# Kernel tuning notes

Measured on AMD Instinct MI355X. Metric: run time of the kernel, lower is better.

## Reference

```python
import jax, jax.numpy as jnp
import numpy as np

D_MODEL = 1024
NUM_HEADS = 16
HEAD_DIM = D_MODEL // NUM_HEADS


def setup_inputs() -> dict:
    key = jax.random.key(0)
    ks = jax.random.split(key, 5)
    s = 0.02
    x = jax.random.normal(ks[0], (4, 2048, D_MODEL), dtype=jnp.float32)
    W_Q = jax.random.normal(ks[1], (D_MODEL, D_MODEL), dtype=jnp.float32) * s
    W_K = jax.random.normal(ks[2], (D_MODEL, D_MODEL), dtype=jnp.float32) * s
    W_V = jax.random.normal(ks[3], (D_MODEL, D_MODEL), dtype=jnp.float32) * s
    W_O = jax.random.normal(ks[4], (D_MODEL, D_MODEL), dtype=jnp.float32) * s
    return {"x": x, "W_Q": W_Q, "W_K": W_K, "W_V": W_V, "W_O": W_O}


def reference(x, W_Q, W_K, W_V, W_O):
    b, s, d = x.shape
    h, hd = NUM_HEADS, HEAD_DIM
    scale = 1.0 / np.sqrt(hd).astype(np.float32)
    # nn.Linear applies x @ W.T; split heads then transpose -> (b, h, s, hd)
    def split(W):
        return (x @ W.T).reshape(b, s, h, hd).transpose(0, 2, 1, 3)
    Q, K, V = split(W_Q), split(W_K), split(W_V)
    scores = jnp.einsum('bhqd,bhkd->bhqk', Q, K) * scale
    causal = jnp.triu(jnp.ones((s, s), dtype=bool), k=1)
    scores = jnp.where(causal, -jnp.inf, scores)
    weights = jax.nn.softmax(scores, axis=-1)
    ctx = jnp.einsum('bhqk,bhkd->bhqd', weights, V)
    ctx = ctx.transpose(0, 2, 1, 3).reshape(b, s, d)
    return ctx @ W_O.T
```

## Files before the change

### kernel.cpp

```cpp
#include <hip/hip_runtime.h>


#define B_  4
#define S_  2048
#define D_  1024
#define H_  16
#define HD_ 64

typedef __attribute__((ext_vector_type(8))) short bf16x8;
typedef __attribute__((ext_vector_type(4))) float f32x4;

#define MFMA16 __builtin_amdgcn_mfma_f32_16x16x32_bf16

__device__ __forceinline__ unsigned short f2b(float f) {
  unsigned u = __builtin_bit_cast(unsigned, f);
  unsigned r = (u + 0x7FFFu + ((u >> 16) & 1u)) >> 16;
  return (unsigned short)r;
}

__device__ __forceinline__ unsigned cvtpk(float lo, float hi) {
  unsigned r;
  asm("v_cvt_pk_bf16_f32 %0, %1, %2" : "=v"(r) : "v"(lo), "v"(hi));
  return r;
}

__device__ __forceinline__ void gll16(const void* g, const void* l) {
  __builtin_amdgcn_global_load_lds(
      (const __attribute__((address_space(1))) unsigned int*)g,
      (__attribute__((address_space(3))) unsigned int*)l, 16, 0, 0);
}

__global__ __launch_bounds__(256) void cvt_all(
    const float4* __restrict__ x,  const float4* __restrict__ wq,
    const float4* __restrict__ wk, const float4* __restrict__ wv,
    const float4* __restrict__ wo,
    ushort4* __restrict__ xb,  ushort4* __restrict__ wqb,
    ushort4* __restrict__ wkb, ushort4* __restrict__ wvb,
    ushort4* __restrict__ wob)
{
  const int y = blockIdx.y;
  const float4* in; ushort4* out;
  if (y < 8)       { in = x  + (size_t)y * 262144; out = xb  + (size_t)y * 262144; }
  else if (y == 8) { in = wq; out = wqb; }
  else if (y == 9) { in = wk; out = wkb; }
  else if (y == 10){ in = wv; out = wvb; }
  else             { in = wo; out = wob; }
  int i = blockIdx.x * 256 + threadIdx.x;
  float4 v = in[i];
  ushort4 o;
  o.x = f2b(v.x); o.y = f2b(v.y); o.z = f2b(v.z); o.w = f2b(v.w);
  out[i] = o;
}

#define GSTG(BF, K0) { \
    _Pragma("unroll") for (int t = 0; t < 2; ++t) { \
      const int grow_ = t*64 + w*16 + srow; \
      const int lbas_ = (t*256 + w*64) * 8; \
      gll16(A + (size_t)(arow + grow_)*1024 + (K0) + scol, &As[BF][lbas_]); \
      gll16(W + (size_t)(brow + grow_)*1024 + (K0) + scol, &Bs[BF][lbas_]); } }

#define GSTEP(BF, SW) { \
    bf16x8 af[4], bfr[4]; \
    _Pragma("unroll") for (int i = 0; i < 4; ++i) \
      af[i]  = *(const bf16x8*)(&As[BF][(wm*64 + i*16 + r16)*32 + rslot]); \
    _Pragma("unroll") for (int i = 0; i < 4; ++i) \
      bfr[i] = *(const bf16x8*)(&Bs[BF][(wn*64 + i*16 + r16)*32 + rslot]); \
    _Pragma("unroll") for (int i = 0; i < 4; ++i) \
      _Pragma("unroll") for (int j = 0; j < 4; ++j) \
        acc[i][j] = (SW) ? MFMA16(bfr[j], af[i], acc[i][j], 0, 0, 0) \
                         : MFMA16(af[i], bfr[j], acc[i][j], 0, 0, 0); }

#define GLOOP(SW) \
  for (int kt = 0; kt < 32; kt += 2) { \
    __syncthreads(); \
    GSTG(1, (kt + 1) * 32); \
    GSTEP(0, SW); \
    __syncthreads(); \
    if (kt + 2 < 32) GSTG(0, (kt + 2) * 32); \
    GSTEP(1, SW); \
  }

template<int MODE>
__global__ __launch_bounds__(256) void gemm_bt(
    const unsigned short* __restrict__ A,
    const unsigned short* __restrict__ W,
    unsigned short* __restrict__ OQ,
    unsigned short* __restrict__ OK,
    unsigned short* __restrict__ OV,
    float* __restrict__ OF)
{
  const int tid  = threadIdx.x;
  const int lane = tid & 63;
  const int w    = tid >> 6;
  const int wm   = w >> 1, wn = w & 1;
  const int r16  = lane & 15, g = lane >> 4;

  const int orig = blockIdx.x + 64 * blockIdx.y;
  const int t_   = orig >> 3;
  const int bm   = (orig & 7) * 8 + (t_ & 7);
  const int bn   = t_ >> 3;

  __shared__ unsigned short As[2][4096];
  __shared__ unsigned short Bs[2][4096];

  const int arow = bm * 128, brow = bn * 128;
  const int srow = lane >> 2;
  const int scol  = ((lane & 3) ^ ((lane >> 3) & 3)) * 8;
  const int rslot = (g ^ ((r16 >> 1) & 3)) * 8;

  f32x4 acc[4][4] = {};
  const bool vblk = (MODE == 0) && (bn >= 16);
  GSTG(0, 0);
  if (!vblk) { GLOOP(true) } else { GLOOP(false) }

  if (MODE == 1) {
    #pragma unroll
    for (int i = 0; i < 4; ++i)
      #pragma unroll
      for (int j = 0; j < 4; ++j) {
        int t = arow + wm*64 + i*16 + r16;
        int f = brow + wn*64 + j*16 + g*4;
        float4 st;
        st.x = acc[i][j][0]; st.y = acc[i][j][1];
        st.z = acc[i][j][2]; st.w = acc[i][j][3];
        *(float4*)(&OF[(size_t)t * 1024 + f]) = st;
      }
  } else if (!vblk) {
    unsigned short* Od = (bn < 8) ? OQ : OK;
    const float scl = (bn < 8) ? 0.18033688f : 1.0f;
    #pragma unroll
    for (int i = 0; i < 4; ++i)
      #pragma unroll
      for (int j = 0; j < 4; ++j) {
        int t = arow + wm*64 + i*16 + r16;
        int f = (brow & 1023) + wn*64 + j*16 + g*4;
        int b = t >> 11, s = t & 2047, h = f >> 6, hd = f & 63;
        uint2 cw;
        cw.x = cvtpk(acc[i][j][0] * scl, acc[i][j][1] * scl);
        cw.y = cvtpk(acc[i][j][2] * scl, acc[i][j][3] * scl);
        *(uint2*)(&Od[((((size_t)b*H_ + h)*S_) + s)*HD_ + hd]) = cw;
      }
  } else {
    #pragma unroll
    for (int i = 0; i < 4; ++i)
      #pragma unroll
      for (int j = 0; j < 4; ++j) {
        int t0 = arow + wm*64 + i*16 + g*4;
        int f  = (brow & 1023) + wn*64 + j*16 + r16;
        int b = t0 >> 11, s = t0 & 2047, h = f >> 6, hd = f & 63;
        uint2 cw;
        cw.x = cvtpk(acc[i][j][0], acc[i][j][1]);
        cw.y = cvtpk(acc[i][j][2], acc[i][j][3]);
        *(uint2*)(&OV[(((size_t)b*H_ + h)*HD_ + hd)*S_ + s]) = cw;
      }
  }
}

#define ASTG(BF, KB) { \
    gll16(Kh + (size_t)((KB) + tr0 +     rsub)*HD_ + csw, &KVb[BF][0][ tr0     *64]); \
    gll16(Kh + (size_t)((KB) + tr0 + 8 + rsub)*HD_ + csw, &KVb[BF][0][(tr0 + 8)*64]); \
    gll16(Vh + (size_t)(tr0 +     rsub)*S_ + (KB) + csw,  &KVb[BF][1][ tr0     *64]); \
    gll16(Vh + (size_t)(tr0 + 8 + rsub)*S_ + (KB) + csw,  &KVb[BF][1][(tr0 + 8)*64]); }

#define ACOMP2(BF, KB) { \
    const int kb_ = (KB); \
    if (kb_ <= qw + 31) { \
      f32x4 sc[2][4]; \
      __builtin_amdgcn_s_setprio(1); \
      _Pragma("unroll") for (int c = 0; c < 4; ++c) { \
        bf16x8 kf0 = *(const bf16x8*)((const char*)&KVb[BF][0][0] + (c*16 + r16)*128 + ((( g      ^ (r16 & 7)) & 7) << 4)); \
        bf16x8 kf1 = *(const bf16x8*)((const char*)&KVb[BF][0][0] + (c*16 + r16)*128 + ((((4 + g) ^ (r16 & 7)) & 7) << 4)); \
        _Pragma("unroll") for (int qi = 0; qi < 2; ++qi) { \
          f32x4 s_ = {}; \
          s_ = MFMA16(kf0, qf[qi][0], s_, 0, 0, 0); \
          s_ = MFMA16(kf1, qf[qi][1], s_, 0, 0, 0); \
          sc[qi][c] = s_; } } \
      __builtin_amdgcn_s_setprio(0); \
      _Pragma("unroll") for (int qi = 0; qi < 2; ++qi) { \
        f32x4 p4[4]; \
        if (kb_ + 63 > qw + qi*16) { \
          const int qrow_ = qw + qi*16 + r16; \
          _Pragma("unroll") for (int c = 0; c < 4; ++c) \
            _Pragma("unroll") for (int r = 0; r < 4; ++r) \
              p4[c][r] = (kb_ + c*16 + g*4 + r > qrow_) ? 0.f : exp2f(sc[qi][c][r]); \
        } else { \
          _Pragma("unroll") for (int c = 0; c < 4; ++c) \
            _Pragma("unroll") for (int r = 0; r < 4; ++r) \
              p4[c][r] = exp2f(sc[qi][c][r]); } \
        char* prp_ = Plw + (qi*16 + r16)*128; \
        const int swz_ = (r16 & 7) << 4; \
        _Pragma("unroll") for (int c = 0; c < 4; ++c) { \
          uint2 pw_; \
          pw_.x = cvtpk(p4[c][0], p4[c][1]); \
          pw_.y = cvtpk(p4[c][2], p4[c][3]); \
          *(uint2*)(prp_ + ((c*32 + g*8) ^ swz_)) = pw_; } } \
      __builtin_amdgcn_s_setprio(1); \
      _Pragma("unroll") for (int kc = 0; kc < 2; ++kc) { \
        bf16x8 pf0_ = *(const bf16x8*)(Plw + r16*128        + ((kc*64 + g*16) ^ ((r16 & 7) << 4))); \
        bf16x8 pf1_ = *(const bf16x8*)(Plw + (16 + r16)*128 + ((kc*64 + g*16) ^ ((r16 & 7) << 4))); \
        oL[0] = MFMA16(onesf, pf0_, oL[0], 0, 0, 0); \
        oL[1] = MFMA16(onesf, pf1_, oL[1], 0, 0, 0); \
        _Pragma("unroll") for (int dn = 0; dn < 4; ++dn) { \
          bf16x8 vf_ = *(const bf16x8*)((const char*)&KVb[BF][1][0] + (dn*16 + r16)*128 + ((((kc*4 + g) ^ (r16 & 7)) & 7) << 4)); \
          oT[0][dn] = MFMA16(vf_, pf0_, oT[0][dn], 0, 0, 0); \
          oT[1][dn] = MFMA16(vf_, pf1_, oT[1][dn], 0, 0, 0); } } \
      __builtin_amdgcn_s_setprio(0); \
    } }

__global__ __launch_bounds__(256, 3) void attn_fwd(
    const unsigned short* __restrict__ Q,
    const unsigned short* __restrict__ K,
    const unsigned short* __restrict__ Vt,
    unsigned short* __restrict__ C)
{
  const int tid  = threadIdx.x;
  const int lane = tid & 63;
  const int w    = tid >> 6;
  const int r16  = lane & 15, g = lane >> 4;

  const int l_   = blockIdx.x;
  const int bh   = (l_ & 7) * 8 + ((l_ >> 3) & 7);
  const int jt   = 15 - (l_ >> 6);
  const int bb   = bh >> 4, hh = bh & 15;

  const unsigned short* Qh = Q  + (size_t)bh * S_ * HD_;
  const unsigned short* Kh = K  + (size_t)bh * S_ * HD_;
  const unsigned short* Vh = Vt + (size_t)bh * HD_ * S_;

  __shared__ unsigned short KVb[2][2][4096];
  __shared__ unsigned short Pl[4][2048];
  char* Plw = (char*)&Pl[w][0];

  const int rsub = lane >> 3;
  const int csw  = ((lane & 7) ^ rsub) * 8;
  const int tr0  = w * 16;

  bf16x8 onesf;
  #pragma unroll
  for (int j = 0; j < 8; ++j) onesf[j] = (short)0x3F80;

  const int q0 = jt * 128;
  const int qw = q0 + w * 32;
  const int nt = 2 * jt + 2;

  bf16x8 qf[2][2];
  #pragma unroll
  for (int qi = 0; qi < 2; ++qi)
    #pragma unroll
    for (int dh = 0; dh < 2; ++dh)
      qf[qi][dh] = *(const bf16x8*)(&Qh[(size_t)(qw + qi*16 + r16) * HD_ + dh*32 + g*8]);

  f32x4 oT[2][4] = {};
  f32x4 oL[2] = {};

  ASTG(0, 0);

  for (int kt = 0; kt < nt; kt += 2) {
    __syncthreads();
    ASTG(1, (kt + 1) * 64);
    ACOMP2(0, kt * 64);
    __syncthreads();
    if (kt + 2 < nt) ASTG(0, (kt + 2) * 64);
    ACOMP2(1, (kt + 1) * 64);
  }

  #pragma unroll
  for (int qi = 0; qi < 2; ++qi) {
    float inv = 1.0f / oL[qi][0];
    int tok = bb * S_ + qw + qi*16 + r16;
    #pragma unroll
    for (int dn = 0; dn < 4; ++dn) {
      uint2 cw;
      cw.x = cvtpk(oT[qi][dn][0] * inv, oT[qi][dn][1] * inv);
      cw.y = cvtpk(oT[qi][dn][2] * inv, oT[qi][dn][3] * inv);
      *(uint2*)(&C[(size_t)tok * D_ + hh*HD_ + dn*16 + g*4]) = cw;
    }
  }
}

extern "C" void kernel_launch(void* const* d_in, const int* in_sizes, int n_in,
                              void* d_out, int out_size, void* d_ws, size_t ws_size,
                              hipStream_t stream) {
  const float* x  = (const float*)d_in[0];
  const float* Wq = (const float*)d_in[1];
  const float* Wk = (const float*)d_in[2];
  const float* Wv = (const float*)d_in[3];
  const float* Wo = (const float*)d_in[4];

  char* ws = (char*)d_ws;
  unsigned short* xb  = (unsigned short*)(ws);
  unsigned short* Wqb = (unsigned short*)(ws + 16777216);
  unsigned short* Wkb = (unsigned short*)(ws + 18874368);
  unsigned short* Wvb = (unsigned short*)(ws + 20971520);
  unsigned short* Wob = (unsigned short*)(ws + 23068672);
  unsigned short* Qb  = (unsigned short*)(ws + 25165824);
  unsigned short* Kb  = (unsigned short*)(ws + 41943040);
  unsigned short* Vtb = (unsigned short*)(ws + 58720256);
  unsigned short* Cb  = (unsigned short*)(ws + 75497472);

  cvt_all<<<dim3(1024, 12), 256, 0, stream>>>(
      (const float4*)x, (const float4*)Wq, (const float4*)Wk,
      (const float4*)Wv, (const float4*)Wo,
      (ushort4*)xb, (ushort4*)Wqb, (ushort4*)Wkb, (ushort4*)Wvb, (ushort4*)Wob);

  gemm_bt<0><<<dim3(64, 24), 256, 0, stream>>>(xb, Wqb, Qb, Kb, Vtb, nullptr);
  attn_fwd<<<1024, 256, 0, stream>>>(Qb, Kb, Vtb, Cb);
  gemm_bt<1><<<dim3(64, 8), 256, 0, stream>>>(Cb, Wob, nullptr, nullptr, nullptr,
                                              (float*)d_out);
}
```

Before: 169.0 us.

## Replace QKV projection with 256x256-tile 8-wave pipelined GEMM kernel

The QKV projection moves to a new kernel with 256x256 output tiles, 512 threads (8 waves), a 64-wide K step, and a quarter-by-quarter schedule that interleaves LDS fragment loads, async global-to-LDS prefetch, explicit vmcnt waits and raw barriers around MFMA bursts at raised priority. It is launched twice: once for Q/K (which relies on Wq/Wk/Wv being contiguous in the workspace) and once for the transposed V output. The aim is more data reuse per loaded tile and better overlap of memory and MFMA work. In exchange it needs 128KB of LDS per block, has high register pressure, depends on hand-tuned wait counts, and the V launch alone has only 128 blocks. The output projection GEMM is split into its own simplified kernel.

```diff
diff --git a/kernel.cpp b/kernel.cpp
--- a/kernel.cpp
+++ b/kernel.cpp
@@ -29,6 +29,10 @@
       (const __attribute__((address_space(1))) unsigned int*)g,
       (__attribute__((address_space(3))) unsigned int*)l, 16, 0, 0);
 }
+
+#define BARF { asm volatile("" ::: "memory"); __builtin_amdgcn_s_barrier(); \
+               asm volatile("" ::: "memory"); }
+#define VMW(N) asm volatile("s_waitcnt vmcnt(" #N ")" ::: "memory")
 
 __global__ __launch_bounds__(256) void cvt_all(
     const float4* __restrict__ x,  const float4* __restrict__ wq,
@@ -52,6 +56,140 @@
   out[i] = o;
 }
 
+#define SGA8(BUF, KT, MH) { \
+    _Pragma("unroll") for (int c_ = 0; c_ < 2; ++c_) { \
+      const int rl_ = aRow0 + c_*8; \
+      gll16(A + (size_t)(arow + rl_ + (MH)*64 + rsub8)*1024 + (KT)*64 + colswz, \
+            &Ah[BUF][(rl_ + (MH)*64)*64]); } }
+
+#define SGB8(BUF, KT, NH) { \
+    _Pragma("unroll") for (int c_ = 0; c_ < 2; ++c_) { \
+      const int rl_ = bRow0 + c_*8; \
+      gll16(W + (size_t)(brow + rl_ + (NH)*32 + rsub8)*1024 + (KT)*64 + colswz, \
+            &Bh[BUF][(rl_ + (NH)*32)*64]); } }
+
+#define LDA8(BUF, MH) { \
+    _Pragma("unroll") for (int mfi_ = 0; mfi_ < 4; ++mfi_) \
+      _Pragma("unroll") for (int ks_ = 0; ks_ < 2; ++ks_) \
+        afr[mfi_][ks_] = *(const bf16x8*)(aB[BUF] + ((MH)*4 + mfi_)*2048 + ks_*64); }
+
+#define LDB8(BUF, NH) { \
+    _Pragma("unroll") for (int nfi_ = 0; nfi_ < 2; ++nfi_) \
+      _Pragma("unroll") for (int ks_ = 0; ks_ < 2; ++ks_) \
+        bfr[nfi_][ks_] = *(const bf16x8*)(bB[BUF] + ((NH)*2 + nfi_)*2048 + ks_*64); }
+
+#define MMQ8(MH, NH) { \
+    __builtin_amdgcn_s_setprio(1); \
+    _Pragma("unroll") for (int mfi_ = 0; mfi_ < 4; ++mfi_) \
+      _Pragma("unroll") for (int nfi_ = 0; nfi_ < 2; ++nfi_) \
+        _Pragma("unroll") for (int ks_ = 0; ks_ < 2; ++ks_) { \
+          if (SW) acc[(MH)*4+mfi_][(NH)*2+nfi_] = \
+            MFMA16(bfr[nfi_][ks_], afr[mfi_][ks_], acc[(MH)*4+mfi_][(NH)*2+nfi_], 0,0,0); \
+          else    acc[(MH)*4+mfi_][(NH)*2+nfi_] = \
+            MFMA16(afr[mfi_][ks_], bfr[nfi_][ks_], acc[(MH)*4+mfi_][(NH)*2+nfi_], 0,0,0); } \
+    __builtin_amdgcn_s_setprio(0); }
+
+#define WIN8(BUF, KT) { \
+     \
+    LDB8(BUF, 0); LDA8(BUF, 0); \
+    if ((KT) + 1 < 16) { SGA8(BUF^1, (KT)+1, 1); SGB8(BUF^1, (KT)+1, 0); } \
+    BARF; MMQ8(0, 0); BARF; \
+     \
+    LDB8(BUF, 1); \
+    if ((KT) + 2 < 16) { SGA8(BUF, (KT)+2, 0); } \
+    BARF; MMQ8(0, 1); BARF; \
+     \
+    LDA8(BUF, 1); \
+    if ((KT) + 2 < 16) { SGB8(BUF, (KT)+2, 1); } \
+    BARF; MMQ8(1, 1); BARF; \
+     \
+    LDB8(BUF, 0); \
+    if ((KT) == 14) { VMW(0); } else { VMW(4); } \
+    BARF; MMQ8(1, 0); BARF; }
+
+template<bool SW>
+__global__ __launch_bounds__(512, 2) void gemm_qkv8(
+    const unsigned short* __restrict__ A,
+    const unsigned short* __restrict__ W,
+    unsigned short* __restrict__ OQ,
+    unsigned short* __restrict__ OK,
+    unsigned short* __restrict__ OV)
+{
+  const int tid  = threadIdx.x;
+  const int lane = tid & 63;
+  const int w8   = tid >> 6;
+  const int wm   = w8 >> 2, wn = w8 & 3;
+  const int r16  = lane & 15, g = lane >> 4;
+  const int rsub8 = lane >> 3;
+
+  const int nbn  = SW ? 8 : 4;
+  const int cpx  = 4 * nbn;
+  const int orig = blockIdx.x;
+  const int swz  = (orig & 7) * cpx + (orig >> 3);
+  const int bm   = swz % 32;
+  const int bn   = swz / 32;
+  const int arow = bm * 256;
+  const int brow = (SW ? 0 : 2048) + bn * 256;
+
+  __shared__ unsigned short Ah[2][16384];
+  __shared__ unsigned short Bh[2][16384];
+
+  const int aRow0  = (w8 >> 2) * 128 + (w8 & 3) * 16;
+  const int bRow0  = (w8 >> 1) * 64  + (w8 & 1) * 16;
+  const int colswz = ((lane & 7) << 3) ^ ((lane & 32) >> 1);
+
+  const int swzrd = (g * 16) ^ ((r16 & 4) << 3);
+  const char* aB[2] = {
+    (const char*)&Ah[0][0] + (wm*128 + r16)*128 + swzrd,
+    (const char*)&Ah[1][0] + (wm*128 + r16)*128 + swzrd };
+  const char* bB[2] = {
+    (const char*)&Bh[0][0] + (wn*64 + r16)*128 + swzrd,
+    (const char*)&Bh[1][0] + (wn*64 + r16)*128 + swzrd };
+
+  f32x4 acc[8][4] = {};
+  bf16x8 afr[4][2], bfr[2][2];
+
+  SGA8(0, 0, 0); SGA8(0, 0, 1); SGB8(0, 0, 0); SGB8(0, 0, 1);
+  SGA8(1, 1, 0); SGB8(1, 1, 1);
+  VMW(4);
+  BARF;
+
+  for (int kt = 0; kt < 16; kt += 2) {
+    WIN8(0, kt);
+    WIN8(1, (kt + 1));
+  }
+
+  if (SW) {
+    unsigned short* Od = (brow < 1024) ? OQ : OK;
+    const float scl = (brow < 1024) ? 0.18033688f : 1.0f;
+    #pragma unroll
+    for (int mf = 0; mf < 8; ++mf)
+      #pragma unroll
+      for (int nf = 0; nf < 4; ++nf) {
+        int t = arow + wm*128 + mf*16 + r16;
+        int f = ((brow + wn*64 + nf*16) & 1023) + g*4;
+        int b = t >> 11, s = t & 2047, h = f >> 6, hd = f & 63;
+        uint2 cw;
+        cw.x = cvtpk(acc[mf][nf][0] * scl, acc[mf][nf][1] * scl);
+        cw.y = cvtpk(acc[mf][nf][2] * scl, acc[mf][nf][3] * scl);
+        *(uint2*)(&Od[((((size_t)b*H_ + h)*S_) + s)*HD_ + hd]) = cw;
+      }
+  } else {
+    #pragma unroll
+    for (int mf = 0; mf < 8; ++mf)
+      #pragma unroll
+      for (int nf = 0; nf < 4; ++nf) {
+        int t0 = arow + wm*128 + mf*16 + g*4;
+        int f  = (brow + wn*64 + nf*16 + r16) & 1023;
+        int b = t0 >> 11, s = t0 & 2047, h = f >> 6, hd = f & 63;
+        uint2 cw;
+        cw.x = cvtpk(acc[mf][nf][0], acc[mf][nf][1]);
+        cw.y = cvtpk(acc[mf][nf][2], acc[mf][nf][3]);
+        *(uint2*)(&OV[(((size_t)b*H_ + h)*HD_ + hd)*S_ + s]) = cw;
+      }
+  }
+}
+
 #define GSTG(BF, K0) { \
     _Pragma("unroll") for (int t = 0; t < 2; ++t) { \
       const int grow_ = t*64 + w*16 + srow; \
@@ -59,7 +197,7 @@
       gll16(A + (size_t)(arow + grow_)*1024 + (K0) + scol, &As[BF][lbas_]); \
       gll16(W + (size_t)(brow + grow_)*1024 + (K0) + scol, &Bs[BF][lbas_]); } }
 
-#define GSTEP(BF, SW) { \
+#define GSTEP(BF) { \
     bf16x8 af[4], bfr[4]; \
     _Pragma("unroll") for (int i = 0; i < 4; ++i) \
       af[i]  = *(const bf16x8*)(&As[BF][(wm*64 + i*16 + r16)*32 + rslot]); \
@@ -67,26 +205,11 @@
       bfr[i] = *(const bf16x8*)(&Bs[BF][(wn*64 + i*16 + r16)*32 + rslot]); \
     _Pragma("unroll") for (int i = 0; i < 4; ++i) \
       _Pragma("unroll") for (int j = 0; j < 4; ++j) \
-        acc[i][j] = (SW) ? MFMA16(bfr[j], af[i], acc[i][j], 0, 0, 0) \
-                         : MFMA16(af[i], bfr[j], acc[i][j], 0, 0, 0); }
-
-#define GLOOP(SW) \
-  for (int kt = 0; kt < 32; kt += 2) { \
-    __syncthreads(); \
-    GSTG(1, (kt + 1) * 32); \
-    GSTEP(0, SW); \
-    __syncthreads(); \
-    if (kt + 2 < 32) GSTG(0, (kt + 2) * 32); \
-    GSTEP(1, SW); \
-  }
-
-template<int MODE>
-__global__ __launch_bounds__(256) void gemm_bt(
+        acc[i][j] = MFMA16(bfr[j], af[i], acc[i][j], 0, 0, 0); }
+
+__global__ __launch_bounds__(256) void gemm_o(
     const unsigned short* __restrict__ A,
     const unsigned short* __restrict__ W,
-    unsigned short* __restrict__ OQ,
-    unsigned short* __restrict__ OK,
-    unsigned short* __restrict__ OV,
     float* __restrict__ OF)
 {
   const int tid  = threadIdx.x;
@@ -109,51 +232,27 @@
   const int rslot = (g ^ ((r16 >> 1) & 3)) * 8;
 
   f32x4 acc[4][4] = {};
-  const bool vblk = (MODE == 0) && (bn >= 16);
   GSTG(0, 0);
-  if (!vblk) { GLOOP(true) } else { GLOOP(false) }
-
-  if (MODE == 1) {
+  for (int kt = 0; kt < 32; kt += 2) {
+    __syncthreads();
+    GSTG(1, (kt + 1) * 32);
+    GSTEP(0);
+    __syncthreads();
+    if (kt + 2 < 32) GSTG(0, (kt + 2) * 32);
+    GSTEP(1);
+  }
+
+  #pragma unroll
+  for (int i = 0; i < 4; ++i)
     #pragma unroll
-    for (int i = 0; i < 4; ++i)
-      #pragma unroll
-      for (int j = 0; j < 4; ++j) {
-        int t = arow + wm*64 + i*16 + r16;
-        int f = brow + wn*64 + j*16 + g*4;
-        float4 st;
-        st.x = acc[i][j][0]; st.y = acc[i][j][1];
-        st.z = acc[i][j][2]; st.w = acc[i][j][3];
-        *(float4*)(&OF[(size_t)t * 1024 + f]) = st;
-      }
-  } else if (!vblk) {
-    unsigned short* Od = (bn < 8) ? OQ : OK;
-    const float scl = (bn < 8) ? 0.18033688f : 1.0f;
-    #pragma unroll
-    for (int i = 0; i < 4; ++i)
-      #pragma unroll
-      for (int j = 0; j < 4; ++j) {
-        int t = arow + wm*64 + i*16 + r16;
-        int f = (brow & 1023) + wn*64 + j*16 + g*4;
-        int b = t >> 11, s = t & 2047, h = f >> 6, hd = f & 63;
-        uint2 cw;
-        cw.x = cvtpk(acc[i][j][0] * scl, acc[i][j][1] * scl);
-        cw.y = cvtpk(acc[i][j][2] * scl, acc[i][j][3] * scl);
-        *(uint2*)(&Od[((((size_t)b*H_ + h)*S_) + s)*HD_ + hd]) = cw;
-      }
-  } else {
-    #pragma unroll
-    for (int i = 0; i < 4; ++i)
-      #pragma unroll
-      for (int j = 0; j < 4; ++j) {
-        int t0 = arow + wm*64 + i*16 + g*4;
-        int f  = (brow & 1023) + wn*64 + j*16 + r16;
-        int b = t0 >> 11, s = t0 & 2047, h = f >> 6, hd = f & 63;
-        uint2 cw;
-        cw.x = cvtpk(acc[i][j][0], acc[i][j][1]);
-        cw.y = cvtpk(acc[i][j][2], acc[i][j][3]);
-        *(uint2*)(&OV[(((size_t)b*H_ + h)*HD_ + hd)*S_ + s]) = cw;
-      }
-  }
+    for (int j = 0; j < 4; ++j) {
+      int t = arow + wm*64 + i*16 + r16;
+      int f = brow + wn*64 + j*16 + g*4;
+      float4 st;
+      st.x = acc[i][j][0]; st.y = acc[i][j][1];
+      st.z = acc[i][j][2]; st.w = acc[i][j][3];
+      *(float4*)(&OF[(size_t)t * 1024 + f]) = st;
+    }
 }
 
 #define ASTG(BF, KB) { \
@@ -303,8 +402,8 @@
       (const float4*)Wv, (const float4*)Wo,
       (ushort4*)xb, (ushort4*)Wqb, (ushort4*)Wkb, (ushort4*)Wvb, (ushort4*)Wob);
 
-  gemm_bt<0><<<dim3(64, 24), 256, 0, stream>>>(xb, Wqb, Qb, Kb, Vtb, nullptr);
+  gemm_qkv8<true><<<256, 512, 0, stream>>>(xb, Wqb, Qb, Kb, nullptr);
+  gemm_qkv8<false><<<128, 512, 0, stream>>>(xb, Wqb, nullptr, nullptr, Vtb);
   attn_fwd<<<1024, 256, 0, stream>>>(Qb, Kb, Vtb, Cb);
-  gemm_bt<1><<<dim3(64, 8), 256, 0, stream>>>(Cb, Wob, nullptr, nullptr, nullptr,
-                                              (float*)d_out);
-}
+  gemm_o<<<dim3(64, 8), 256, 0, stream>>>(Cb, Wob, (float*)d_out);
+}
```

After: 187.3 us. 10.8% more time.

## Rebalance GEMM grids: 1024-block QKV with tile loop, 128x64 tiles for O-proj

Applied to the files above, without the earlier changes.

The QKV projection now launches 1024 blocks instead of 1536. The first 512 blocks each compute two 128x128 tiles and the rest compute one, which targets a block count matched to the CU count and avoids a partial final wave. The output projection moves to 128x64 tiles, doubling its grid from 512 to 1024 blocks to fill more CUs, at the cost of less reuse per block. The tradeoff is load imbalance in the QKV kernel and extra A-operand traffic in the O GEMM.

```diff
diff --git a/kernel.cpp b/kernel.cpp
--- a/kernel.cpp
+++ b/kernel.cpp
@@ -80,13 +80,93 @@
     GSTEP(1, SW); \
   }
 
-template<int MODE>
-__global__ __launch_bounds__(256) void gemm_bt(
+__global__ __launch_bounds__(256) void gemm_qkv(
     const unsigned short* __restrict__ A,
     const unsigned short* __restrict__ W,
     unsigned short* __restrict__ OQ,
     unsigned short* __restrict__ OK,
-    unsigned short* __restrict__ OV,
+    unsigned short* __restrict__ OV)
+{
+  const int tid  = threadIdx.x;
+  const int lane = tid & 63;
+  const int w    = tid >> 6;
+  const int wm   = w >> 1, wn = w & 1;
+  const int r16  = lane & 15, g = lane >> 4;
+
+  const int p      = blockIdx.x + 64 * blockIdx.y;
+  const int ntile  = (p < 512) ? 2 : 1;
+
+  __shared__ unsigned short As[2][4096];
+  __shared__ unsigned short Bs[2][4096];
+
+  const int srow = lane >> 2;
+  const int scol  = ((lane & 3) ^ ((lane >> 3) & 3)) * 8;
+  const int rslot = (g ^ ((r16 >> 1) & 3)) * 8;
+
+  for (int tt = 0; tt < ntile; ++tt) {
+    const int tile = tt ? (1024 + p) : p;
+    const int t_  = tile >> 3;
+    const int bm  = (tile & 7) * 8 + (t_ & 7);
+    const int bn  = t_ >> 3;
+    const int arow = bm * 128, brow = bn * 128;
+
+    f32x4 acc[4][4] = {};
+    const bool vblk = (bn >= 16);
+    GSTG(0, 0);
+    if (!vblk) { GLOOP(true) } else { GLOOP(false) }
+
+    if (!vblk) {
+      unsigned short* Od = (bn < 8) ? OQ : OK;
+      const float scl = (bn < 8) ? 0.18033688f : 1.0f;
+      #pragma unroll
+      for (int i = 0; i < 4; ++i)
+        #pragma unroll
+        for (int j = 0; j < 4; ++j) {
+          int t = arow + wm*64 + i*16 + r16;
+          int f = (brow & 1023) + wn*64 + j*16 + g*4;
+          int b = t >> 11, s = t & 2047, h = f >> 6, hd = f & 63;
+          uint2 cw;
+          cw.x = cvtpk(acc[i][j][0] * scl, acc[i][j][1] * scl);
+          cw.y = cvtpk(acc[i][j][2] * scl, acc[i][j][3] * scl);
+          *(uint2*)(&Od[((((size_t)b*H_ + h)*S_) + s)*HD_ + hd]) = cw;
+        }
+    } else {
+      #pragma unroll
+      for (int i = 0; i < 4; ++i)
+        #pragma unroll
+        for (int j = 0; j < 4; ++j) {
+          int t0 = arow + wm*64 + i*16 + g*4;
+          int f  = (brow & 1023) + wn*64 + j*16 + r16;
+          int b = t0 >> 11, s = t0 & 2047, h = f >> 6, hd = f & 63;
+          uint2 cw;
+          cw.x = cvtpk(acc[i][j][0], acc[i][j][1]);
+          cw.y = cvtpk(acc[i][j][2], acc[i][j][3]);
+          *(uint2*)(&OV[(((size_t)b*H_ + h)*HD_ + hd)*S_ + s]) = cw;
+        }
+    }
+  }
+}
+
+#define OSTG(BF, K0) { \
+    _Pragma("unroll") for (int t = 0; t < 2; ++t) { \
+      const int grow_ = t*64 + w*16 + srow; \
+      const int lbas_ = (t*256 + w*64) * 8; \
+      gll16(A + (size_t)(arow + grow_)*1024 + (K0) + scol, &As[BF][lbas_]); } \
+    gll16(W + (size_t)(brow + w*16 + srow)*1024 + (K0) + scol, &Bs[BF][w*512]); }
+
+#define OSTEP(BF) { \
+    bf16x8 af[4], bfr[2]; \
+    _Pragma("unroll") for (int i = 0; i < 4; ++i) \
+      af[i]  = *(const bf16x8*)(&As[BF][(wm*64 + i*16 + r16)*32 + rslot]); \
+    _Pragma("unroll") for (int j = 0; j < 2; ++j) \
+      bfr[j] = *(const bf16x8*)(&Bs[BF][(wn*32 + j*16 + r16)*32 + rslot]); \
+    _Pragma("unroll") for (int i = 0; i < 4; ++i) \
+      _Pragma("unroll") for (int j = 0; j < 2; ++j) \
+        acc[i][j] = MFMA16(bfr[j], af[i], acc[i][j], 0, 0, 0); }
+
+__global__ __launch_bounds__(256) void gemm_o(
+    const unsigned short* __restrict__ A,
+    const unsigned short* __restrict__ W,
     float* __restrict__ OF)
 {
   const int tid  = threadIdx.x;
@@ -101,59 +181,35 @@
   const int bn   = t_ >> 3;
 
   __shared__ unsigned short As[2][4096];
-  __shared__ unsigned short Bs[2][4096];
-
-  const int arow = bm * 128, brow = bn * 128;
+  __shared__ unsigned short Bs[2][2048];
+
+  const int arow = bm * 128, brow = bn * 64;
   const int srow = lane >> 2;
   const int scol  = ((lane & 3) ^ ((lane >> 3) & 3)) * 8;
   const int rslot = (g ^ ((r16 >> 1) & 3)) * 8;
 
-  f32x4 acc[4][4] = {};
-  const bool vblk = (MODE == 0) && (bn >= 16);
-  GSTG(0, 0);
-  if (!vblk) { GLOOP(true) } else { GLOOP(false) }
-
-  if (MODE == 1) {
+  f32x4 acc[4][2] = {};
+  OSTG(0, 0);
+  for (int kt = 0; kt < 32; kt += 2) {
+    __syncthreads();
+    OSTG(1, (kt + 1) * 32);
+    OSTEP(0);
+    __syncthreads();
+    if (kt + 2 < 32) OSTG(0, (kt + 2) * 32);
+    OSTEP(1);
+  }
+
+  #pragma unroll
+  for (int i = 0; i < 4; ++i)
     #pragma unroll
-    for (int i = 0; i < 4; ++i)
-      #pragma unroll
-      for (int j = 0; j < 4; ++j) {
-        int t = arow + wm*64 + i*16 + r16;
-        int f = brow + wn*64 + j*16 + g*4;
-        float4 st;
-        st.x = acc[i][j][0]; st.y = acc[i][j][1];
-        st.z = acc[i][j][2]; st.w = acc[i][j][3];
-        *(float4*)(&OF[(size_t)t * 1024 + f]) = st;
-      }
-  } else if (!vblk) {
-    unsigned short* Od = (bn < 8) ? OQ : OK;
-    const float scl = (bn < 8) ? 0.18033688f : 1.0f;
-    #pragma unroll
-    for (int i = 0; i < 4; ++i)
-      #pragma unroll
-      for (int j = 0; j < 4; ++j) {
-        int t = arow + wm*64 + i*16 + r16;
-        int f = (brow & 1023) + wn*64 + j*16 + g*4;
-        int b = t >> 11, s = t & 2047, h = f >> 6, hd = f & 63;
-        uint2 cw;
-        cw.x = cvtpk(acc[i][j][0] * scl, acc[i][j][1] * scl);
-        cw.y = cvtpk(acc[i][j][2] * scl, acc[i][j][3] * scl);
-        *(uint2*)(&Od[((((size_t)b*H_ + h)*S_) + s)*HD_ + hd]) = cw;
-      }
-  } else {
-    #pragma unroll
-    for (int i = 0; i < 4; ++i)
-      #pragma unroll
-      for (int j = 0; j < 4; ++j) {
-        int t0 = arow + wm*64 + i*16 + g*4;
-        int f  = (brow & 1023) + wn*64 + j*16 + r16;
-        int b = t0 >> 11, s = t0 & 2047, h = f >> 6, hd = f & 63;
-        uint2 cw;
-        cw.x = cvtpk(acc[i][j][0], acc[i][j][1]);
-        cw.y = cvtpk(acc[i][j][2], acc[i][j][3]);
-        *(uint2*)(&OV[(((size_t)b*H_ + h)*HD_ + hd)*S_ + s]) = cw;
-      }
-  }
+    for (int j = 0; j < 2; ++j) {
+      int t = arow + wm*64 + i*16 + r16;
+      int f = brow + wn*32 + j*16 + g*4;
+      float4 st;
+      st.x = acc[i][j][0]; st.y = acc[i][j][1];
+      st.z = acc[i][j][2]; st.w = acc[i][j][3];
+      *(float4*)(&OF[(size_t)t * 1024 + f]) = st;
+    }
 }
 
 #define ASTG(BF, KB) { \
@@ -303,8 +359,7 @@
       (const float4*)Wv, (const float4*)Wo,
       (ushort4*)xb, (ushort4*)Wqb, (ushort4*)Wkb, (ushort4*)Wvb, (ushort4*)Wob);
 
-  gemm_bt<0><<<dim3(64, 24), 256, 0, stream>>>(xb, Wqb, Qb, Kb, Vtb, nullptr);
+  gemm_qkv<<<dim3(64, 16), 256, 0, stream>>>(xb, Wqb, Qb, Kb, Vtb);
   attn_fwd<<<1024, 256, 0, stream>>>(Qb, Kb, Vtb, Cb);
-  gemm_bt<1><<<dim3(64, 8), 256, 0, stream>>>(Cb, Wob, nullptr, nullptr, nullptr,
-                                              (float*)d_out);
-}
+  gemm_o<<<dim3(64, 16), 256, 0, stream>>>(Cb, Wob, (float*)d_out);
+}
```

New measurement: 180.5 us. 1.07x slower.
